# Optimization experiments

Hardware: AMD Instinct MI355X
Metric: run time of the kernel (lower is better)

Reference implementation:

```python
import jax, jax.numpy as jnp
import numpy as np

GRID = 32  # hard-coded voxel resolution in the original module


def setup_inputs() -> dict:
    key = jax.random.key(0)
    k1, k2 = jax.random.split(key)
    points = jax.random.normal(k1, (4, 100000, 3), dtype=jnp.float32)
    features = jax.random.normal(k2, (4, 100000, 64), dtype=jnp.float32)
    return {"points": points, "features": features}


def reference(points, features):
    # points: [B, N, 3], features: [B, N, F]
    B, N, _ = points.shape
    Fdim = features.shape[-1]
    # Global (over whole tensor) min/max normalization, exactly as original
    pmin = points.min()
    pmax = points.max()
    normed = (points - pmin) / (pmax - pmin + 1e-6)  # in [0, 1)
    # torch: (normed // (1/32)).long() == floor(normed * 32)
    vox = jnp.floor(normed * GRID).astype(jnp.int32)  # [B, N, 3], values in [0, 31]
    gidx = vox[..., 0] * (GRID * GRID) + vox[..., 1] * GRID + vox[..., 2]  # [B, N]
    # Scatter-max into a zero-initialized grid (zeros init == implicit max with 0,
    # matching the original torch.zeros output_grid).
    grid = jnp.zeros((B, GRID ** 3, Fdim), dtype=features.dtype)
    batch_ids = jnp.arange(B, dtype=jnp.int32)[:, None]  # [B, 1] broadcast over N
    grid = grid.at[batch_ids, gidx].max(features)
    return grid.reshape(B, GRID, GRID, GRID, Fdim)
```

## Files before the change

### kernel.cpp

```cpp
#include <hip/hip_runtime.h>

#define SPATIAL 32768
#define NBINS   131072
#define FDIM    64

__device__ __forceinline__ unsigned int enc_f32(float f) {
    unsigned int u = __float_as_uint(f);
    return (u & 0x80000000u) ? ~u : (u | 0x80000000u);
}
__device__ __forceinline__ float dec_f32(unsigned int u) {
    u = (u & 0x80000000u) ? (u ^ 0x80000000u) : ~u;
    return __uint_as_float(u);
}

__global__ void init_ws_kernel(unsigned int* mm) {
    mm[0] = 0xFFFFFFFFu;
    mm[1] = 0u;
}

__global__ void minmax_kernel(const float4* __restrict__ pts4, int n4,
                              unsigned int* __restrict__ mm) {
    float lmin = INFINITY, lmax = -INFINITY;
    for (int i = blockIdx.x * blockDim.x + threadIdx.x; i < n4;
         i += gridDim.x * blockDim.x) {
        float4 v = pts4[i];
        lmin = fminf(fminf(lmin, v.x), fminf(v.y, v.z)); lmin = fminf(lmin, v.w);
        lmax = fmaxf(fmaxf(lmax, v.x), fmaxf(v.y, v.z)); lmax = fmaxf(lmax, v.w);
    }
    __shared__ float smin[256], smax[256];
    smin[threadIdx.x] = lmin;
    smax[threadIdx.x] = lmax;
    __syncthreads();
    for (int s = 128; s > 0; s >>= 1) {
        if (threadIdx.x < (unsigned)s) {
            smin[threadIdx.x] = fminf(smin[threadIdx.x], smin[threadIdx.x + s]);
            smax[threadIdx.x] = fmaxf(smax[threadIdx.x], smax[threadIdx.x + s]);
        }
        __syncthreads();
    }
    if (threadIdx.x == 0) {
        atomicMin(&mm[0], enc_f32(smin[0]));
        atomicMax(&mm[1], enc_f32(smax[0]));
    }
}

__global__ void bincount_kernel(const float* __restrict__ pts,
                                const unsigned int* __restrict__ mm,
                                unsigned int* __restrict__ counts,
                                unsigned int* __restrict__ binof,
                                int ntot, int N) {
    int p = blockIdx.x * blockDim.x + threadIdx.x;
    if (p >= ntot) return;
    float pmin = dec_f32(mm[0]);
    float pmax = dec_f32(mm[1]);
    float denom = pmax - pmin + 1e-6f;

    float x = pts[p * 3 + 0];
    float y = pts[p * 3 + 1];
    float z = pts[p * 3 + 2];
    int vx = (int)floorf(((x - pmin) / denom) * 32.0f);
    int vy = (int)floorf(((y - pmin) / denom) * 32.0f);
    int vz = (int)floorf(((z - pmin) / denom) * 32.0f);
    vx = min(max(vx, 0), 31);
    vy = min(max(vy, 0), 31);
    vz = min(max(vz, 0), 31);
    int b = p / N;
    unsigned int bin = (unsigned)b * SPATIAL + vx * 1024 + vy * 32 + vz;
    binof[p] = bin;
    atomicAdd(&counts[bin], 1u);
}

__global__ void scan_blocksums_kernel(const unsigned int* __restrict__ counts,
                                      unsigned int* __restrict__ bsum) {
    __shared__ unsigned int s[256];
    int i = blockIdx.x * 256 + threadIdx.x;
    s[threadIdx.x] = counts[i];
    __syncthreads();
    for (int st = 128; st > 0; st >>= 1) {
        if (threadIdx.x < (unsigned)st) s[threadIdx.x] += s[threadIdx.x + st];
        __syncthreads();
    }
    if (threadIdx.x == 0) bsum[blockIdx.x] = s[0];
}

__global__ void scan_top_kernel(unsigned int* __restrict__ bsum,
                                unsigned int* __restrict__ boff) {
    __shared__ unsigned int s[512];
    unsigned int v = bsum[threadIdx.x];
    s[threadIdx.x] = v;
    __syncthreads();
    for (int st = 1; st < 512; st <<= 1) {
        unsigned int add = (threadIdx.x >= (unsigned)st) ? s[threadIdx.x - st] : 0u;
        __syncthreads();
        s[threadIdx.x] += add;
        __syncthreads();
    }
    boff[threadIdx.x] = s[threadIdx.x] - v;
}

__global__ void scan_write_kernel(const unsigned int* __restrict__ counts,
                                  const unsigned int* __restrict__ boff,
                                  unsigned int* __restrict__ offsets,
                                  unsigned int* __restrict__ cursor) {
    __shared__ unsigned int s[256];
    int i = blockIdx.x * 256 + threadIdx.x;
    unsigned int v = counts[i];
    s[threadIdx.x] = v;
    __syncthreads();
    for (int st = 1; st < 256; st <<= 1) {
        unsigned int add = (threadIdx.x >= (unsigned)st) ? s[threadIdx.x - st] : 0u;
        __syncthreads();
        s[threadIdx.x] += add;
        __syncthreads();
    }
    unsigned int off = boff[blockIdx.x] + s[threadIdx.x] - v;
    offsets[i] = off;
    cursor[i] = off;
}

__global__ void build_order_kernel(const unsigned int* __restrict__ binof,
                                   unsigned int* __restrict__ cursor,
                                   unsigned int* __restrict__ order,
                                   int ntot) {
    int p = blockIdx.x * blockDim.x + threadIdx.x;
    if (p >= ntot) return;
    unsigned int bin = binof[p];
    unsigned int pos = atomicAdd(&cursor[bin], 1u);
    order[pos] = (unsigned)p;
}

__global__ void gather_kernel(const float* __restrict__ feat,
                              const unsigned int* __restrict__ counts,
                              const unsigned int* __restrict__ offsets,
                              const unsigned int* __restrict__ order,
                              float* __restrict__ out) {
    int gtid = blockIdx.x * blockDim.x + threadIdx.x;
    int bin = gtid >> 6;
    int lane = threadIdx.x & 63;
    if (bin >= NBINS) return;

    unsigned int cnt = counts[bin];
    unsigned int off = offsets[bin];

    float m = 0.0f;
    unsigned int i = 0;
    while (i < cnt) {
        unsigned int nb = min(64u, cnt - i);
        int idx = (lane < (int)nb) ? (int)order[off + i + lane] : 0;

        unsigned int j = 0;
        for (; j + 16 <= nb; j += 16) {
            float f[16];
#pragma unroll
            for (int k = 0; k < 16; ++k) {
                int p = __shfl(idx, (int)(j + k), 64);
                f[k] = feat[(size_t)p * FDIM + lane];
            }
#pragma unroll
            for (int k = 0; k < 16; ++k) m = fmaxf(m, f[k]);
        }
        for (; j + 4 <= nb; j += 4) {
            float f[4];
#pragma unroll
            for (int k = 0; k < 4; ++k) {
                int p = __shfl(idx, (int)(j + k), 64);
                f[k] = feat[(size_t)p * FDIM + lane];
            }
#pragma unroll
            for (int k = 0; k < 4; ++k) m = fmaxf(m, f[k]);
        }
        for (; j < nb; ++j) {
            int p = __shfl(idx, (int)j, 64);
            m = fmaxf(m, feat[(size_t)p * FDIM + lane]);
        }
        i += nb;
    }
    out[(size_t)bin * FDIM + lane] = m;
}

__global__ void scatter_kernel(const float* __restrict__ pts,
                               const float* __restrict__ feat,
                               const unsigned int* __restrict__ mm,
                               unsigned int* __restrict__ out,
                               int ntot, int N) {
    int lane = threadIdx.x & 63;
    int p = blockIdx.x * 4 + (threadIdx.x >> 6);
    if (p >= ntot) return;
    float pmin = dec_f32(mm[0]);
    float pmax = dec_f32(mm[1]);
    float denom = pmax - pmin + 1e-6f;
    float x = pts[p * 3 + 0], y = pts[p * 3 + 1], z = pts[p * 3 + 2];
    int vx = (int)floorf(((x - pmin) / denom) * 32.0f);
    int vy = (int)floorf(((y - pmin) / denom) * 32.0f);
    int vz = (int)floorf(((z - pmin) / denom) * 32.0f);
    vx = min(max(vx, 0), 31);
    vy = min(max(vy, 0), 31);
    vz = min(max(vz, 0), 31);
    int gidx = vx * 1024 + vy * 32 + vz;
    int b = p / N;
    float f = feat[(size_t)p * FDIM + lane];
    if (f > 0.0f) {
        atomicMax(out + ((size_t)b * SPATIAL + gidx) * FDIM + lane,
                  __float_as_uint(f));
    }
}

extern "C" void kernel_launch(void* const* d_in, const int* in_sizes, int n_in,
                              void* d_out, int out_size, void* d_ws, size_t ws_size,
                              hipStream_t stream) {
    const float* pts = (const float*)d_in[0];
    const float* feat = (const float*)d_in[1];

    int npts3 = in_sizes[0];
    int ntot = npts3 / 3;
    int B = out_size / (SPATIAL * FDIM);
    int N = ntot / B;

    unsigned int* ws = (unsigned int*)d_ws;
    unsigned int* counts  = ws;
    unsigned int* cursor  = ws + NBINS;
    unsigned int* offsets = ws + 2 * NBINS;
    unsigned int* binof   = ws + 3 * NBINS;
    unsigned int* order   = binof + ntot;
    unsigned int* mm      = order + ntot;
    unsigned int* bsum    = mm + 2;
    unsigned int* boff    = bsum + 512;

    size_t need = ((size_t)3 * NBINS + 2 * (size_t)ntot + 2 + 1024) * 4;
    if (ws_size < need) {
        unsigned int* mm2 = ws;
        hipLaunchKernelGGL(init_ws_kernel, dim3(1), dim3(1), 0, stream, mm2);
        hipLaunchKernelGGL(minmax_kernel, dim3(512), dim3(256), 0, stream,
                           (const float4*)pts, npts3 / 4, mm2);
        hipMemsetAsync(d_out, 0, (size_t)out_size * sizeof(float), stream);
        hipLaunchKernelGGL(scatter_kernel, dim3((ntot + 3) / 4), dim3(256), 0,
                           stream, pts, feat, mm2, (unsigned int*)d_out, ntot, N);
        return;
    }

    hipMemsetAsync(counts, 0, (size_t)NBINS * 4, stream);
    hipLaunchKernelGGL(init_ws_kernel, dim3(1), dim3(1), 0, stream, mm);
    hipLaunchKernelGGL(minmax_kernel, dim3(512), dim3(256), 0, stream,
                       (const float4*)pts, npts3 / 4, mm);
    int pblocks = (ntot + 255) / 256;
    hipLaunchKernelGGL(bincount_kernel, dim3(pblocks), dim3(256), 0, stream,
                       pts, mm, counts, binof, ntot, N);
    hipLaunchKernelGGL(scan_blocksums_kernel, dim3(NBINS / 256), dim3(256), 0,
                       stream, counts, bsum);
    hipLaunchKernelGGL(scan_top_kernel, dim3(1), dim3(512), 0, stream,
                       bsum, boff);
    hipLaunchKernelGGL(scan_write_kernel, dim3(NBINS / 256), dim3(256), 0,
                       stream, counts, boff, offsets, cursor);
    hipLaunchKernelGGL(build_order_kernel, dim3(pblocks), dim3(256), 0, stream,
                       binof, cursor, order, ntot);
    hipLaunchKernelGGL(gather_kernel, dim3(NBINS * 64 / 256), dim3(256), 0,
                       stream, feat, counts, offsets, order, (float*)d_out);
}
```

Measured before the change: 275.0 us.

## Replace three-pass scan with single-pass atomic compaction and gather only non-empty bins

The three scan kernels become one compaction kernel that uses wave ballots and shuffles plus global atomics to assign bins their offsets and to list the non-empty bins. The gather kernel becomes persistent and visits only the listed bins, so output rows for empty bins are covered by a memset of the whole output instead. Max initialisation now uses a complemented encoding so that a single memset of 0xFF sets up both values, which removes the init kernel. Offsets are no longer in bin order, but since each bin is reduced independently the results stay correct. The cost is an extra full-output memset and atomic contention on two counters.

```diff
diff --git a/kernel.cpp b/kernel.cpp
--- a/kernel.cpp
+++ b/kernel.cpp
@@ -13,10 +13,6 @@
     return __uint_as_float(u);
 }
 
-__global__ void init_ws_kernel(unsigned int* mm) {
-    mm[0] = 0xFFFFFFFFu;
-    mm[1] = 0u;
-}
 
 __global__ void minmax_kernel(const float4* __restrict__ pts4, int n4,
                               unsigned int* __restrict__ mm) {
@@ -40,7 +36,7 @@
     }
     if (threadIdx.x == 0) {
         atomicMin(&mm[0], enc_f32(smin[0]));
-        atomicMax(&mm[1], enc_f32(smax[0]));
+        atomicMin(&mm[1], ~enc_f32(smax[0]));
     }
 }
 
@@ -52,7 +48,7 @@
     int p = blockIdx.x * blockDim.x + threadIdx.x;
     if (p >= ntot) return;
     float pmin = dec_f32(mm[0]);
-    float pmax = dec_f32(mm[1]);
+    float pmax = dec_f32(~mm[1]);
     float denom = pmax - pmin + 1e-6f;
 
     float x = pts[p * 3 + 0];
@@ -70,52 +66,50 @@
     atomicAdd(&counts[bin], 1u);
 }
 
-__global__ void scan_blocksums_kernel(const unsigned int* __restrict__ counts,
-                                      unsigned int* __restrict__ bsum) {
-    __shared__ unsigned int s[256];
+__global__ void compact_kernel(const unsigned int* __restrict__ counts,
+                               unsigned int* __restrict__ nlist,
+                               unsigned int* __restrict__ tail,
+                               unsigned int* __restrict__ nebins,
+                               unsigned int* __restrict__ offsets,
+                               unsigned int* __restrict__ cursor) {
     int i = blockIdx.x * 256 + threadIdx.x;
-    s[threadIdx.x] = counts[i];
+    unsigned int cnt = counts[i];
+    int lane = threadIdx.x & 63;
+    int wid = threadIdx.x >> 6;
+    bool flag = cnt > 0;
+
+    unsigned long long mask = __ballot(flag);
+    unsigned int fpre = __popcll(mask & ((1ULL << lane) - 1ULL));
+    unsigned int ftot = __popcll(mask);
+
+    unsigned int cscan = cnt;
+#pragma unroll
+    for (int d = 1; d < 64; d <<= 1) {
+        unsigned int v = __shfl_up(cscan, (unsigned)d, 64);
+        if (lane >= d) cscan += v;
+    }
+    unsigned int cpre = cscan - cnt;
+    unsigned int ctot = __shfl(cscan, 63, 64);
+
+    __shared__ unsigned int wf[4], wc[4], base[2];
+    if (lane == 0) { wf[wid] = ftot; wc[wid] = ctot; }
     __syncthreads();
-    for (int st = 128; st > 0; st >>= 1) {
-        if (threadIdx.x < (unsigned)st) s[threadIdx.x] += s[threadIdx.x + st];
-        __syncthreads();
-    }
-    if (threadIdx.x == 0) bsum[blockIdx.x] = s[0];
-}
-
-__global__ void scan_top_kernel(unsigned int* __restrict__ bsum,
-                                unsigned int* __restrict__ boff) {
-    __shared__ unsigned int s[512];
-    unsigned int v = bsum[threadIdx.x];
-    s[threadIdx.x] = v;
+    unsigned int bf = 0, bc = 0;
+    for (int w = 0; w < wid; ++w) { bf += wf[w]; bc += wc[w]; }
+    if (threadIdx.x == 0) {
+        unsigned int tf = wf[0] + wf[1] + wf[2] + wf[3];
+        unsigned int tc = wc[0] + wc[1] + wc[2] + wc[3];
+        base[0] = atomicAdd(nlist, tf);
+        base[1] = atomicAdd(tail, tc);
+    }
     __syncthreads();
-    for (int st = 1; st < 512; st <<= 1) {
-        unsigned int add = (threadIdx.x >= (unsigned)st) ? s[threadIdx.x - st] : 0u;
-        __syncthreads();
-        s[threadIdx.x] += add;
-        __syncthreads();
-    }
-    boff[threadIdx.x] = s[threadIdx.x] - v;
-}
-
-__global__ void scan_write_kernel(const unsigned int* __restrict__ counts,
-                                  const unsigned int* __restrict__ boff,
-                                  unsigned int* __restrict__ offsets,
-                                  unsigned int* __restrict__ cursor) {
-    __shared__ unsigned int s[256];
-    int i = blockIdx.x * 256 + threadIdx.x;
-    unsigned int v = counts[i];
-    s[threadIdx.x] = v;
-    __syncthreads();
-    for (int st = 1; st < 256; st <<= 1) {
-        unsigned int add = (threadIdx.x >= (unsigned)st) ? s[threadIdx.x - st] : 0u;
-        __syncthreads();
-        s[threadIdx.x] += add;
-        __syncthreads();
-    }
-    unsigned int off = boff[blockIdx.x] + s[threadIdx.x] - v;
-    offsets[i] = off;
-    cursor[i] = off;
+    if (flag) {
+        unsigned int pos = base[0] + bf + fpre;
+        unsigned int off = base[1] + bc + cpre;
+        nebins[pos] = (unsigned)i;
+        offsets[i] = off;
+        cursor[i] = off;
+    }
 }
 
 __global__ void build_order_kernel(const unsigned int* __restrict__ binof,
@@ -133,51 +127,60 @@
                               const unsigned int* __restrict__ counts,
                               const unsigned int* __restrict__ offsets,
                               const unsigned int* __restrict__ order,
+                              const unsigned int* __restrict__ nebins,
+                              const unsigned int* __restrict__ nlist,
                               float* __restrict__ out) {
-    int gtid = blockIdx.x * blockDim.x + threadIdx.x;
-    int bin = gtid >> 6;
     int lane = threadIdx.x & 63;
-    if (bin >= NBINS) return;
-
-    unsigned int cnt = counts[bin];
-    unsigned int off = offsets[bin];
-
-    float m = 0.0f;
-    unsigned int i = 0;
-    while (i < cnt) {
-        unsigned int nb = min(64u, cnt - i);
-        int idx = (lane < (int)nb) ? (int)order[off + i + lane] : 0;
-
-        unsigned int j = 0;
-        for (; j + 16 <= nb; j += 16) {
-            float f[16];
-#pragma unroll
-            for (int k = 0; k < 16; ++k) {
-                int p = __shfl(idx, (int)(j + k), 64);
-                f[k] = feat[(size_t)p * FDIM + lane];
+    unsigned int wave = (blockIdx.x * blockDim.x + threadIdx.x) >> 6;
+    unsigned int nwaves = (gridDim.x * blockDim.x) >> 6;
+    unsigned int nl = *nlist;
+
+    for (unsigned int li = wave; li < nl; li += nwaves) {
+        unsigned int bin = nebins[li];
+        unsigned int cnt = counts[bin];
+        unsigned int off = offsets[bin];
+
+        float m = 0.0f;
+        unsigned int i = 0;
+        while (i < cnt) {
+            unsigned int nb = min(64u, cnt - i);
+            int idx = (lane < (int)nb) ? (int)order[off + i + lane] : 0;
+
+            unsigned int j = 0;
+            for (; j + 16 <= nb; j += 16) {
+                float f[16];
+#pragma unroll
+                for (int k = 0; k < 16; ++k) {
+                    int p = __shfl(idx, (int)(j + k), 64);
+                    f[k] = feat[(size_t)p * FDIM + lane];
+                }
+#pragma unroll
+                for (int k = 0; k < 16; ++k) m = fmaxf(m, f[k]);
             }
-#pragma unroll
-            for (int k = 0; k < 16; ++k) m = fmaxf(m, f[k]);
+            for (; j + 4 <= nb; j += 4) {
+                float f[4];
+#pragma unroll
+                for (int k = 0; k < 4; ++k) {
+                    int p = __shfl(idx, (int)(j + k), 64);
+                    f[k] = feat[(size_t)p * FDIM + lane];
+                }
+#pragma unroll
+                for (int k = 0; k < 4; ++k) m = fmaxf(m, f[k]);
+            }
+            for (; j < nb; ++j) {
+                int p = __shfl(idx, (int)j, 64);
+                m = fmaxf(m, feat[(size_t)p * FDIM + lane]);
+            }
+            i += nb;
         }
-        for (; j + 4 <= nb; j += 4) {
-            float f[4];
-#pragma unroll
-            for (int k = 0; k < 4; ++k) {
-                int p = __shfl(idx, (int)(j + k), 64);
-                f[k] = feat[(size_t)p * FDIM + lane];
-            }
-#pragma unroll
-            for (int k = 0; k < 4; ++k) m = fmaxf(m, f[k]);
-        }
-        for (; j < nb; ++j) {
-            int p = __shfl(idx, (int)j, 64);
-            m = fmaxf(m, feat[(size_t)p * FDIM + lane]);
-        }
-        i += nb;
-    }
-    out[(size_t)bin * FDIM + lane] = m;
-}
-
+        out[(size_t)bin * FDIM + lane] = m;
+    }
+}
+
+__global__ void init_mm_kernel(unsigned int* mm) {
+    mm[0] = 0xFFFFFFFFu;
+    mm[1] = 0xFFFFFFFFu;
+}
 __global__ void scatter_kernel(const float* __restrict__ pts,
                                const float* __restrict__ feat,
                                const unsigned int* __restrict__ mm,
@@ -187,7 +190,7 @@
     int p = blockIdx.x * 4 + (threadIdx.x >> 6);
     if (p >= ntot) return;
     float pmin = dec_f32(mm[0]);
-    float pmax = dec_f32(mm[1]);
+    float pmax = dec_f32(~mm[1]);
     float denom = pmax - pmin + 1e-6f;
     float x = pts[p * 3 + 0], y = pts[p * 3 + 1], z = pts[p * 3 + 2];
     int vx = (int)floorf(((x - pmin) / denom) * 32.0f);
@@ -218,18 +221,19 @@
 
     unsigned int* ws = (unsigned int*)d_ws;
     unsigned int* counts  = ws;
-    unsigned int* cursor  = ws + NBINS;
-    unsigned int* offsets = ws + 2 * NBINS;
-    unsigned int* binof   = ws + 3 * NBINS;
+    unsigned int* nlist   = ws + NBINS;
+    unsigned int* tail    = ws + NBINS + 1;
+    unsigned int* mm      = ws + NBINS + 2;
+    unsigned int* cursor  = ws + NBINS + 4;
+    unsigned int* offsets = ws + 2 * NBINS + 4;
+    unsigned int* nebins  = ws + 3 * NBINS + 4;
+    unsigned int* binof   = ws + 4 * NBINS + 4;
     unsigned int* order   = binof + ntot;
-    unsigned int* mm      = order + ntot;
-    unsigned int* bsum    = mm + 2;
-    unsigned int* boff    = bsum + 512;
-
-    size_t need = ((size_t)3 * NBINS + 2 * (size_t)ntot + 2 + 1024) * 4;
+
+    size_t need = ((size_t)4 * NBINS + 4 + 2 * (size_t)ntot) * 4;
     if (ws_size < need) {
         unsigned int* mm2 = ws;
-        hipLaunchKernelGGL(init_ws_kernel, dim3(1), dim3(1), 0, stream, mm2);
+        hipLaunchKernelGGL(init_mm_kernel, dim3(1), dim3(1), 0, stream, mm2);
         hipLaunchKernelGGL(minmax_kernel, dim3(512), dim3(256), 0, stream,
                            (const float4*)pts, npts3 / 4, mm2);
         hipMemsetAsync(d_out, 0, (size_t)out_size * sizeof(float), stream);
@@ -238,21 +242,20 @@
         return;
     }
 
-    hipMemsetAsync(counts, 0, (size_t)NBINS * 4, stream);
-    hipLaunchKernelGGL(init_ws_kernel, dim3(1), dim3(1), 0, stream, mm);
+    hipMemsetAsync(counts, 0, ((size_t)NBINS + 2) * 4, stream);
+    hipMemsetAsync(mm, 0xFF, 8, stream);
+    hipMemsetAsync(d_out, 0, (size_t)out_size * sizeof(float), stream);
+
     hipLaunchKernelGGL(minmax_kernel, dim3(512), dim3(256), 0, stream,
                        (const float4*)pts, npts3 / 4, mm);
     int pblocks = (ntot + 255) / 256;
     hipLaunchKernelGGL(bincount_kernel, dim3(pblocks), dim3(256), 0, stream,
                        pts, mm, counts, binof, ntot, N);
-    hipLaunchKernelGGL(scan_blocksums_kernel, dim3(NBINS / 256), dim3(256), 0,
-                       stream, counts, bsum);
-    hipLaunchKernelGGL(scan_top_kernel, dim3(1), dim3(512), 0, stream,
-                       bsum, boff);
-    hipLaunchKernelGGL(scan_write_kernel, dim3(NBINS / 256), dim3(256), 0,
-                       stream, counts, boff, offsets, cursor);
+    hipLaunchKernelGGL(compact_kernel, dim3(NBINS / 256), dim3(256), 0, stream,
+                       counts, nlist, tail, nebins, offsets, cursor);
     hipLaunchKernelGGL(build_order_kernel, dim3(pblocks), dim3(256), 0, stream,
                        binof, cursor, order, ntot);
-    hipLaunchKernelGGL(gather_kernel, dim3(NBINS * 64 / 256), dim3(256), 0,
-                       stream, feat, counts, offsets, order, (float*)d_out);
-}
+    hipLaunchKernelGGL(gather_kernel, dim3(1024), dim3(256), 0, stream,
+                       feat, counts, offsets, order, nebins, nlist,
+                       (float*)d_out);
+}
```

New measurement: 273.4 us. No clear change (-0.6%).
